# Kernel optimization log

Hardware: AMD Instinct MI355X
Metric: run time of the kernel (lower is better)

## Reference

```python
import jax, jax.numpy as jnp
import numpy as np

B, S, D, H = 2, 2048, 768, 12
N = D // H  # head dim = 64
NEG = -1e12


def setup_inputs() -> dict:
    key = jax.random.key(0)
    ks = jax.random.split(key, 6)
    scale = 1.0 / np.sqrt(D)
    return {
        "inputs": jax.random.normal(ks[0], (B, S, D), dtype=jnp.float32),
        "masks": jnp.ones((B, S), dtype=jnp.int32),
        "Wq": jax.random.normal(ks[1], (D, D), dtype=jnp.float32) * scale,
        "bq": jnp.zeros((D,), dtype=jnp.float32),
        "Wk": jax.random.normal(ks[2], (D, D), dtype=jnp.float32) * scale,
        "bk": jnp.zeros((D,), dtype=jnp.float32),
        "Wv": jax.random.normal(ks[3], (D, D), dtype=jnp.float32) * scale,
        "bv": jnp.zeros((D,), dtype=jnp.float32),
        "Wo": jax.random.normal(ks[4], (D, D), dtype=jnp.float32) * scale,
        "bo": jnp.zeros((D,), dtype=jnp.float32),
    }


def reference(inputs, masks, Wq, bq, Wk, bk, Wv, bv, Wo, bo):
    # projections: [B,S,D] -> [B,H,S,N]
    def proj(x, W, b):
        y = jnp.einsum('bsd,df->bsf', x, W) + b
        return y.reshape(B, -1, H, N).transpose(0, 2, 1, 3)

    q = proj(inputs, Wq, bq)
    k = proj(inputs, Wk, bk)
    v = proj(inputs, Wv, bv)

    # scores [B,H,S,S]
    a = jnp.einsum('bhqn,bhkn->bhqk', q, k) / jnp.float32(np.sqrt(N))
    m = masks[:, None, None, :]  # [B,1,1,S]
    a = jnp.where(m == 0, jnp.float32(NEG), a)
    a = jax.nn.softmax(a, axis=-1)

    o = jnp.einsum('bhqk,bhkn->bhqn', a, v)  # [B,H,S,N]
    o = o.transpose(0, 2, 1, 3).reshape(B, -1, H * N)
    return jnp.einsum('bsd,df->bsf', o, Wo) + bo
```

## Files before the change

### kernel.cpp

```cpp
#include <hip/hip_runtime.h>
#include <hip/hip_bf16.h>

#define B_ 2
#define S_ 2048
#define D_ 768
#define H_ 12
#define BS_ (B_*S_)
#define NEGL2 -1.44e12f
#define SCALE2 0.18033688f

typedef __bf16 bf16;
typedef __attribute__((ext_vector_type(8))) __bf16 bf16x8;
typedef __attribute__((ext_vector_type(4))) float f32x4;
typedef __attribute__((ext_vector_type(16))) float f32x16;

__global__ __launch_bounds__(256) void cast_f32_bf16(const float* __restrict__ in,
                                                     bf16* __restrict__ out, int n) {
    int i = (blockIdx.x * 256 + threadIdx.x) * 8;
    if (i + 8 <= n) {
        float4 a = *(const float4*)(in + i);
        float4 b = *(const float4*)(in + i + 4);
        bf16x8 v;
        v[0] = (bf16)a.x; v[1] = (bf16)a.y; v[2] = (bf16)a.z; v[3] = (bf16)a.w;
        v[4] = (bf16)b.x; v[5] = (bf16)b.y; v[6] = (bf16)b.z; v[7] = (bf16)b.w;
        *(bf16x8*)(out + i) = v;
    }
}

__global__ __launch_bounds__(256) void transpose_w4(const float* __restrict__ W0,
                                                    const float* __restrict__ W1,
                                                    const float* __restrict__ W2,
                                                    const float* __restrict__ W3,
                                                    bf16* __restrict__ Wt0) {
    const float* Ws[4] = {W0, W1, W2, W3};
    const float* W = Ws[blockIdx.z];
    bf16* Wt = Wt0 + (size_t)blockIdx.z * D_ * D_;
    __shared__ float tile[16][17];
    int bx = blockIdx.x, by = blockIdx.y;
    int tx = threadIdx.x & 15, ty = threadIdx.x >> 4;
    tile[ty][tx] = W[(by * 16 + ty) * D_ + bx * 16 + tx];
    __syncthreads();
    Wt[(bx * 16 + ty) * D_ + by * 16 + tx] = (bf16)tile[tx][ty];
}

__device__ inline unsigned pk2(float a, float b) {
    union { unsigned u; __bf16 h[2]; } x;
    x.h[0] = (__bf16)a; x.h[1] = (__bf16)b;
    return x.u;
}

__device__ __forceinline__ void gload16(const void* g, void* l) {
    __builtin_amdgcn_global_load_lds(
        (const __attribute__((address_space(1))) unsigned int*)g,
        (__attribute__((address_space(3))) unsigned int*)l, 16, 0, 0);
}

__global__ __launch_bounds__(256) void gemm_qkv(const bf16* __restrict__ A,
                                                const bf16* __restrict__ Bt,
                                                const float* __restrict__ bq,
                                                const float* __restrict__ bk,
                                                const float* __restrict__ bv,
                                                bf16* __restrict__ Qo,
                                                bf16* __restrict__ Ko,
                                                bf16* __restrict__ Vo) {
    constexpr int K = 768;
    __shared__ __align__(16) bf16 As[64 * 64];
    __shared__ __align__(16) bf16 Bs[128 * 64];
    const int bm = blockIdx.x, bn = blockIdx.y;
    const int t = threadIdx.x;
    const int lane = t & 63, wid = t >> 6;
    const int wm = wid >> 1, wn = wid & 1;
    f32x4 acc[2][4] = {};

    const char* gA = (const char*)(A + (size_t)(bm * 64) * K);
    const char* gB = (const char*)(Bt + (size_t)(bn * 128) * K);
    const int srow = wid * 8 + (lane >> 3);
    const int chg = ((lane & 7) ^ (lane >> 3)) * 16;

    for (int kt = 0; kt < 12; ++kt) {
        __syncthreads();
#pragma unroll
        for (int c = 0; c < 2; ++c)
            gload16(gA + (size_t)(c * 32 + srow) * (K * 2) + kt * 128 + chg,
                    (char*)As + c * 4096 + wid * 1024);
#pragma unroll
        for (int c = 0; c < 4; ++c)
            gload16(gB + (size_t)(c * 32 + srow) * (K * 2) + kt * 128 + chg,
                    (char*)Bs + c * 4096 + wid * 1024);
        asm volatile("s_waitcnt vmcnt(0)");
        __syncthreads();

#pragma unroll
        for (int kb = 0; kb < 2; ++kb) {
            const int chunk = ((kb * 4 + (lane >> 4)) ^ (lane & 7)) * 16;
            bf16x8 aF[2], bF[4];
#pragma unroll
            for (int mf = 0; mf < 2; ++mf)
                aF[mf] = *(const bf16x8*)((const char*)As + (wm * 32 + mf * 16 + (lane & 15)) * 128 + chunk);
#pragma unroll
            for (int nf = 0; nf < 4; ++nf)
                bF[nf] = *(const bf16x8*)((const char*)Bs + (wn * 64 + nf * 16 + (lane & 15)) * 128 + chunk);
#pragma unroll
            for (int mf = 0; mf < 2; ++mf)
#pragma unroll
                for (int nf = 0; nf < 4; ++nf)
                    acc[mf][nf] = __builtin_amdgcn_mfma_f32_16x16x32_bf16(aF[mf], bF[nf], acc[mf][nf], 0, 0, 0);
        }
    }

    const int mid = bn / 6;
    const float* bias = (mid == 0) ? bq : (mid == 1) ? bk : bv;
#pragma unroll
    for (int mf = 0; mf < 2; ++mf) {
#pragma unroll
        for (int nf = 0; nf < 4; ++nf) {
#pragma unroll
            for (int r = 0; r < 4; ++r) {
                int row = bm * 64 + wm * 32 + mf * 16 + (lane >> 4) * 4 + r;
                int lc = (bn - mid * 6) * 128 + wn * 64 + nf * 16 + (lane & 15);
                float v = acc[mf][nf][r] + bias[lc];
                if (mid == 0) {
                    Qo[(size_t)row * D_ + lc] = (bf16)(v * SCALE2);
                } else if (mid == 1) {
                    Ko[(size_t)row * D_ + lc] = (bf16)v;
                } else {
                    int bb = row >> 11, s = row & 2047, hh = lc >> 6, nn = lc & 63;
                    Vo[(size_t)(((bb * H_ + hh) << 6) + nn) * S_ + s] = (bf16)v;
                }
            }
        }
    }
}

__global__ __launch_bounds__(256) void gemm_out(const bf16* __restrict__ A,
                                                const bf16* __restrict__ Bt,
                                                const float* __restrict__ bias,
                                                float* __restrict__ Cout) {
    constexpr int K = 768;
    __shared__ __align__(16) bf16 As[32 * 64];
    __shared__ __align__(16) bf16 Bs[128 * 64];
    const int bm = blockIdx.x, bn = blockIdx.y;
    const int t = threadIdx.x;
    const int lane = t & 63, wid = t >> 6;
    const int wm = wid >> 1, wn = wid & 1;
    f32x4 acc[4] = {};

    const char* gA = (const char*)(A + (size_t)(bm * 32) * K);
    const char* gB = (const char*)(Bt + (size_t)(bn * 128) * K);
    const int srow = wid * 8 + (lane >> 3);
    const int chg = ((lane & 7) ^ (lane >> 3)) * 16;

    for (int kt = 0; kt < 12; ++kt) {
        __syncthreads();
        gload16(gA + (size_t)srow * (K * 2) + kt * 128 + chg,
                (char*)As + wid * 1024);
#pragma unroll
        for (int c = 0; c < 4; ++c)
            gload16(gB + (size_t)(c * 32 + srow) * (K * 2) + kt * 128 + chg,
                    (char*)Bs + c * 4096 + wid * 1024);
        asm volatile("s_waitcnt vmcnt(0)");
        __syncthreads();

#pragma unroll
        for (int kb = 0; kb < 2; ++kb) {
            const int chunk = ((kb * 4 + (lane >> 4)) ^ (lane & 7)) * 16;
            bf16x8 aF = *(const bf16x8*)((const char*)As + (wm * 16 + (lane & 15)) * 128 + chunk);
            bf16x8 bF[4];
#pragma unroll
            for (int nf = 0; nf < 4; ++nf)
                bF[nf] = *(const bf16x8*)((const char*)Bs + (wn * 64 + nf * 16 + (lane & 15)) * 128 + chunk);
#pragma unroll
            for (int nf = 0; nf < 4; ++nf)
                acc[nf] = __builtin_amdgcn_mfma_f32_16x16x32_bf16(aF, bF[nf], acc[nf], 0, 0, 0);
        }
    }

#pragma unroll
    for (int nf = 0; nf < 4; ++nf)
#pragma unroll
        for (int r = 0; r < 4; ++r) {
            int row = bm * 32 + wm * 16 + (lane >> 4) * 4 + r;
            int col = bn * 128 + wn * 64 + nf * 16 + (lane & 15);
            Cout[(size_t)row * D_ + col] = acc[nf][r] + bias[col];
        }
}

__global__ __launch_bounds__(256, 3) void attn_fwd10(const bf16* __restrict__ Qs,
                                                     const bf16* __restrict__ Kg,
                                                     const bf16* __restrict__ Vt,
                                                     const int* __restrict__ masks,
                                                     bf16* __restrict__ Oa) {
    __shared__ __align__(16) char Sbuf[2][16384];
    __shared__ float Lr[2][64];

    const int qt = blockIdx.x, bh = blockIdx.y;
    const int b = bh / H_, h = bh % H_;
    const int t = threadIdx.x;
    const int lane = t & 63, w = t >> 6;
    const int lo = lane & 31, hi = lane >> 5;
    const int half = w >> 1;
    const int qs = w & 1;
    const int role = w & 1;

    unsigned long long mflags;
    {
        const int* mb = masks + b * S_ + half * 1024 + lane * 16;
        int anyz = 0;
#pragma unroll
        for (int u = 0; u < 4; ++u) {
            int4 mv = *(const int4*)(mb + u * 4);
            anyz |= (!mv.x) | (!mv.y) | (!mv.z) | (!mv.w);
        }
        mflags = __ballot(anyz != 0);
    }

    bf16x8 bQ[4];
    {
        const bf16* qp = Qs + (size_t)(b * S_ + qt * 64 + qs * 32 + lo) * D_ + h * 64 + 8 * hi;
#pragma unroll
        for (int kb = 0; kb < 4; ++kb) bQ[kb] = *(const bf16x8*)(qp + 16 * kb);
    }

    const int srow = lane >> 3;
    const int scolS = ((lane & 7) * 16) ^ ((srow & 7) << 4);
    const char* gsrc;
    size_t cstride, tstep;
    if (role == 0) {
        gsrc = (const char*)Kg + ((size_t)(b * S_ + half * 1024 + srow) * D_ + h * 64) * 2 + scolS;
        cstride = (size_t)8 * D_ * 2;
        tstep = (size_t)64 * D_ * 2;
    } else {
        gsrc = (const char*)Vt + ((size_t)(bh * 64 + srow) * S_ + half * 1024) * 2 + scolS;
        cstride = (size_t)8 * S_ * 2;
        tstep = 128;
    }
    char* dst = &Sbuf[half][0] + role * 8192 + lane * 16;
    const char* Kh = &Sbuf[half][0];
    const char* Vh = Kh + 8192;

    bf16x8 sreg[8];
#pragma unroll
    for (int j = 0; j < 8; ++j) sreg[j] = *(const bf16x8*)(gsrc + j * cstride);

    f32x16 oo[2] = {};
    float lrun = 0.f;

#pragma unroll 1
    for (int kt = 0; kt < 16; ++kt) {
        __syncthreads();
#pragma unroll
        for (int j = 0; j < 8; ++j) *(bf16x8*)(dst + j * 1024) = sreg[j];
        __syncthreads();
        if (kt < 15) {
            const char* p = gsrc + (size_t)(kt + 1) * tstep;
#pragma unroll
            for (int j = 0; j < 8; ++j) sreg[j] = *(const bf16x8*)(p + j * cstride);
        }

        const bool mk = (mflags >> (4 * kt)) & 0xFULL;
        float lsum = 0.f;
#pragma unroll
        for (int kb2 = 0; kb2 < 2; ++kb2) {
            const int row = kb2 * 32 + lo;
            const int rsw = (row & 7) << 4;
            f32x16 sa = {};
            __builtin_amdgcn_s_setprio(1);
#pragma unroll
            for (int kb = 0; kb < 4; ++kb) {
                bf16x8 aK = *(const bf16x8*)(Kh + row * 128 + ((kb * 32 + hi * 16) ^ rsw));
                sa = __builtin_amdgcn_mfma_f32_32x32x16_bf16(aK, bQ[kb], sa, 0, 0, 0);
            }
            __builtin_amdgcn_s_setprio(0);
            float pp[16];
            if (!mk) {
#pragma unroll
                for (int r = 0; r < 16; ++r) pp[r] = __builtin_amdgcn_exp2f(sa[r]);
            } else {
#pragma unroll
                for (int r = 0; r < 16; ++r) {
                    int kv = half * 1024 + kt * 64 + kb2 * 32 + (r & 3) + 8 * (r >> 2) + 4 * hi;
                    float madd = masks[b * S_ + kv] ? 0.f : NEGL2;
                    pp[r] = __builtin_amdgcn_exp2f(sa[r] + madd);
                }
            }
            float s8[8];
#pragma unroll
            for (int i = 0; i < 8; ++i) s8[i] = pp[i] + pp[i + 8];
            lsum += ((s8[0] + s8[1]) + (s8[2] + s8[3])) + ((s8[4] + s8[5]) + (s8[6] + s8[7]));

#pragma unroll
            for (int ks2 = 0; ks2 < 2; ++ks2) {
                const float* q8 = pp + ks2 * 8;
                unsigned u0 = pk2(q8[0], q8[1]);
                unsigned u1 = pk2(q8[2], q8[3]);
                unsigned u2 = pk2(q8[4], q8[5]);
                unsigned u3 = pk2(q8[6], q8[7]);
                asm("v_permlane32_swap_b32 %0, %1" : "+v"(u0), "+v"(u2));
                asm("v_permlane32_swap_b32 %0, %1" : "+v"(u1), "+v"(u3));
                union { unsigned u[4]; bf16x8 v; } pa;
                pa.u[0] = u0; pa.u[1] = u1; pa.u[2] = u2; pa.u[3] = u3;
                const int ks = kb2 * 2 + ks2;
                __builtin_amdgcn_s_setprio(1);
#pragma unroll
                for (int nb = 0; nb < 2; ++nb) {
                    const int vr = nb * 32 + lo;
                    bf16x8 aV = *(const bf16x8*)(Vh + vr * 128 +
                                                 ((ks * 32 + hi * 16) ^ ((vr & 7) << 4)));
                    oo[nb] = __builtin_amdgcn_mfma_f32_32x32x16_bf16(aV, pa.v, oo[nb], 0, 0, 0);
                }
                __builtin_amdgcn_s_setprio(0);
            }
        }
        lrun += lsum + __shfl_xor(lsum, 32, 64);
    }

    __syncthreads();
    float* mbuf = (float*)&Sbuf[0][0];
    if (w >= 2) {
        float* d = mbuf + qs * 2048;
#pragma unroll
        for (int nb = 0; nb < 2; ++nb)
#pragma unroll
            for (int r = 0; r < 16; ++r)
                d[(nb * 16 + r) * 64 + lane] = oo[nb][r];
        Lr[qs][lane] = lrun;
    }
    __syncthreads();
    if (w < 2) {
        const float* s = mbuf + qs * 2048;
#pragma unroll
        for (int nb = 0; nb < 2; ++nb)
#pragma unroll
            for (int r = 0; r < 16; ++r)
                oo[nb][r] += s[(nb * 16 + r) * 64 + lane];
        float inv = 1.f / (lrun + Lr[qs][lane]);

        char* ot = (char*)&Sbuf[1][0] + qs * 8192;
#pragma unroll
        for (int nb = 0; nb < 2; ++nb)
#pragma unroll
            for (int tq = 0; tq < 4; ++tq) {
                int n0 = tq * 8 + hi * 4 + nb * 32;
                *(unsigned*)(ot + lo * 144 + n0 * 2) =
                    pk2(oo[nb][tq * 4 + 0] * inv, oo[nb][tq * 4 + 1] * inv);
                *(unsigned*)(ot + lo * 144 + n0 * 2 + 4) =
                    pk2(oo[nb][tq * 4 + 2] * inv, oo[nb][tq * 4 + 3] * inv);
            }
#pragma unroll
        for (int pass = 0; pass < 4; ++pass) {
            int chunk = hi + pass * 2;
            bf16x8 vv = *(const bf16x8*)(ot + lo * 144 + chunk * 16);
            *(bf16x8*)(Oa + (size_t)(b * S_ + qt * 64 + qs * 32 + lo) * D_ + h * 64 + chunk * 8) = vv;
        }
    }
}

extern "C" void kernel_launch(void* const* d_in, const int* in_sizes, int n_in,
                              void* d_out, int out_size, void* d_ws, size_t ws_size,
                              hipStream_t stream) {
    (void)in_sizes; (void)n_in; (void)out_size; (void)ws_size;
    const float* x  = (const float*)d_in[0];
    const int* masks = (const int*)d_in[1];
    const float* Wq = (const float*)d_in[2];
    const float* bq = (const float*)d_in[3];
    const float* Wk = (const float*)d_in[4];
    const float* bk = (const float*)d_in[5];
    const float* Wv = (const float*)d_in[6];
    const float* bv = (const float*)d_in[7];
    const float* Wo = (const float*)d_in[8];
    const float* bo = (const float*)d_in[9];
    float* out = (float*)d_out;

    char* ws = (char*)d_ws;
    size_t off = 0;
    auto alloc = [&](size_t bytes) {
        void* p = ws + off;
        off += (bytes + 255) & ~(size_t)255;
        return p;
    };
    bf16* Xb  = (bf16*)alloc((size_t)BS_ * D_ * 2);
    bf16* Wqt = (bf16*)alloc((size_t)D_ * D_ * 2);
    bf16* Wkt = (bf16*)alloc((size_t)D_ * D_ * 2);
    bf16* Wvt = (bf16*)alloc((size_t)D_ * D_ * 2);
    bf16* Wot = (bf16*)alloc((size_t)D_ * D_ * 2);
    bf16* Qb  = (bf16*)alloc((size_t)BS_ * D_ * 2);
    bf16* Kb2 = (bf16*)alloc((size_t)BS_ * D_ * 2);
    bf16* Vtb = (bf16*)alloc((size_t)BS_ * D_ * 2);
    bf16* Ab  = (bf16*)alloc((size_t)BS_ * D_ * 2);
    (void)Wkt; (void)Wvt;

    cast_f32_bf16<<<(BS_ * D_) / 2048, 256, 0, stream>>>(x, Xb, BS_ * D_);
    transpose_w4<<<dim3(48, 48, 4), 256, 0, stream>>>(Wq, Wk, Wv, Wo, Wqt);

    gemm_qkv<<<dim3(64, 18), 256, 0, stream>>>(Xb, Wqt, bq, bk, bv, Qb, Kb2, Vtb);

    attn_fwd10<<<dim3(32, 24), 256, 0, stream>>>(Qb, Kb2, Vtb, masks, Ab);

    gemm_out<<<dim3(128, 6), 256, 0, stream>>>(Ab, Wot, bo, out);
}
```

Baseline: 99.78 us.

## Register-prefetch next K tile in projection GEMMs instead of direct-to-LDS loads

Replaces the global_load_lds direct-to-LDS copies in the QKV and output projection GEMMs with register-staged loads. The loads for tile kt+1 are issued before the MFMA work on tile kt, then written to LDS at the start of the next iteration. This is meant to hide global memory latency behind compute, where before each iteration stalled on vmcnt(0). It costs extra VGPRs and explicit LDS stores, and keeps a single LDS buffer with two barriers per iteration.

```diff
diff --git a/kernel.cpp b/kernel.cpp
--- a/kernel.cpp
+++ b/kernel.cpp
@@ -47,12 +47,6 @@
     union { unsigned u; __bf16 h[2]; } x;
     x.h[0] = (__bf16)a; x.h[1] = (__bf16)b;
     return x.u;
-}
-
-__device__ __forceinline__ void gload16(const void* g, void* l) {
-    __builtin_amdgcn_global_load_lds(
-        (const __attribute__((address_space(1))) unsigned int*)g,
-        (__attribute__((address_space(3))) unsigned int*)l, 16, 0, 0);
 }
 
 __global__ __launch_bounds__(256) void gemm_qkv(const bf16* __restrict__ A,
@@ -76,19 +70,29 @@
     const char* gB = (const char*)(Bt + (size_t)(bn * 128) * K);
     const int srow = wid * 8 + (lane >> 3);
     const int chg = ((lane & 7) ^ (lane >> 3)) * 16;
+    char* dA = (char*)As + wid * 1024 + lane * 16;
+    char* dB = (char*)Bs + wid * 1024 + lane * 16;
+
+    bf16x8 sA[2], sB[4];
+    auto LOADG = [&](int kt) {
+#pragma unroll
+        for (int c = 0; c < 2; ++c)
+            sA[c] = *(const bf16x8*)(gA + (size_t)(c * 32 + srow) * (K * 2) + kt * 128 + chg);
+#pragma unroll
+        for (int c = 0; c < 4; ++c)
+            sB[c] = *(const bf16x8*)(gB + (size_t)(c * 32 + srow) * (K * 2) + kt * 128 + chg);
+    };
+
+    LOADG(0);
 
     for (int kt = 0; kt < 12; ++kt) {
         __syncthreads();
 #pragma unroll
-        for (int c = 0; c < 2; ++c)
-            gload16(gA + (size_t)(c * 32 + srow) * (K * 2) + kt * 128 + chg,
-                    (char*)As + c * 4096 + wid * 1024);
-#pragma unroll
-        for (int c = 0; c < 4; ++c)
-            gload16(gB + (size_t)(c * 32 + srow) * (K * 2) + kt * 128 + chg,
-                    (char*)Bs + c * 4096 + wid * 1024);
-        asm volatile("s_waitcnt vmcnt(0)");
-        __syncthreads();
+        for (int c = 0; c < 2; ++c) *(bf16x8*)(dA + c * 4096) = sA[c];
+#pragma unroll
+        for (int c = 0; c < 4; ++c) *(bf16x8*)(dB + c * 4096) = sB[c];
+        __syncthreads();
+        if (kt < 11) LOADG(kt + 1);
 
 #pragma unroll
         for (int kb = 0; kb < 2; ++kb) {
@@ -149,17 +153,26 @@
     const char* gB = (const char*)(Bt + (size_t)(bn * 128) * K);
     const int srow = wid * 8 + (lane >> 3);
     const int chg = ((lane & 7) ^ (lane >> 3)) * 16;
+    char* dA = (char*)As + wid * 1024 + lane * 16;
+    char* dB = (char*)Bs + wid * 1024 + lane * 16;
+
+    bf16x8 sA, sB[4];
+    auto LOADG = [&](int kt) {
+        sA = *(const bf16x8*)(gA + (size_t)srow * (K * 2) + kt * 128 + chg);
+#pragma unroll
+        for (int c = 0; c < 4; ++c)
+            sB[c] = *(const bf16x8*)(gB + (size_t)(c * 32 + srow) * (K * 2) + kt * 128 + chg);
+    };
+
+    LOADG(0);
 
     for (int kt = 0; kt < 12; ++kt) {
         __syncthreads();
-        gload16(gA + (size_t)srow * (K * 2) + kt * 128 + chg,
-                (char*)As + wid * 1024);
-#pragma unroll
-        for (int c = 0; c < 4; ++c)
-            gload16(gB + (size_t)(c * 32 + srow) * (K * 2) + kt * 128 + chg,
-                    (char*)Bs + c * 4096 + wid * 1024);
-        asm volatile("s_waitcnt vmcnt(0)");
-        __syncthreads();
+        *(bf16x8*)dA = sA;
+#pragma unroll
+        for (int c = 0; c < 4; ++c) *(bf16x8*)(dB + c * 4096) = sB[c];
+        __syncthreads();
+        if (kt < 11) LOADG(kt + 1);
 
 #pragma unroll
         for (int kb = 0; kb < 2; ++kb) {
```

After: 103.5 us. 1.04x slower.
